# Kernel tuning notes

Measured on AMD Instinct MI355X. Metric: run time of the kernel, lower is better.

Reference implementation:

```python
import jax, jax.numpy as jnp
import numpy as np

B, S, E = 2, 4096, 1024
QD, VD = 64, 64
WIN, DIL = 5, 2


def setup_inputs() -> dict:
    key = jax.random.key(0)
    ks = jax.random.split(key, 7)
    sc = E ** -0.5  # linear-layer init scale
    return {
        "x": jax.random.normal(ks[0], (B, S, E), jnp.float32),
        "Wq": jax.random.normal(ks[1], (E, QD), jnp.float32) * sc,
        "bq": jnp.zeros((QD,), jnp.float32),
        "Wk": jax.random.normal(ks[2], (E, QD), jnp.float32) * sc,
        "bk": jnp.zeros((QD,), jnp.float32),
        "Wv": jax.random.normal(ks[3], (E, VD), jnp.float32) * sc,
        "bv": jnp.zeros((VD,), jnp.float32),
    }


def reference(x, Wq, bq, Wk, bk, Wv, bv):
    b, s, _ = x.shape
    Q = x @ Wq + bq  # (b, s, QD)
    K = x @ Wk + bk  # (b, s, QD)
    V = x @ Wv + bv  # (b, s, VD)

    half = WIN // 2
    offsets = DIL * (jnp.arange(WIN) - half)
    i = jnp.arange(s)                                  # (s,)
    j = i[None, :] + offsets[:, None]
    valid = (j >= 0) & (j < s)                         # in-range band entries
    jc = jnp.clip(j, 0, s - 1)

    Kg = K[:, jc, :]
    # per-offset diagonal dot products Q_i . K_{i+d}
    c = jnp.einsum('bsd,bwsd->bws', Q, Kg) * valid

    ib = jnp.broadcast_to(i[None, :], (WIN, s))
    # Banded score matrix, zeros off-band (as in the original: torch.zeros scatter).
    # Masked (invalid) entries add 0, so clipped index collisions are harmless.
    scores = jnp.zeros((b, s, s), x.dtype).at[:, ib, jc].add(c)

    attn = jax.nn.softmax(scores, axis=2)              # softmax over full row incl. zeros
    return attn @ V                                    # (b, s, VD)
```

## Files before the change

### kernel.cpp

```cpp
#include <hip/hip_runtime.h>
#include <hip/hip_bf16.h>

typedef __hip_bfloat16 bf16;
typedef short bf16x8 __attribute__((ext_vector_type(8)));
typedef float f32x4 __attribute__((ext_vector_type(4)));

#define S_LEN 4096
#define NBATCH 2
#define EDIM 1024
#define DDIM 64
#define MROWS (NBATCH * S_LEN)

#define GLOBAL_AS __attribute__((address_space(1)))
#define LDS_AS __attribute__((address_space(3)))

union frag_u { bf16x8 v; bf16 e[8]; };

__device__ __forceinline__ void async_ld16(const void* gp, void* lp) {
  __builtin_amdgcn_global_load_lds((const GLOBAL_AS void*)gp,
                                   (LDS_AS void*)lp, 16, 0, 0);
}

__device__ __forceinline__ void cvt_split(const float4& a, const float4& b,
                                          bf16x8& hi, bf16x8& lo) {
  float v[8] = {a.x, a.y, a.z, a.w, b.x, b.y, b.z, b.w};
  frag_u h, l;
#pragma unroll
  for (int e = 0; e < 8; e++) {
    bf16 hh = __float2bfloat16(v[e]);
    h.e[e] = hh;
    l.e[e] = __float2bfloat16(v[e] - __bfloat162float(hh));
  }
  hi = h.v;
  lo = l.v;
}

__global__ __launch_bounds__(256) void pack_w_kernel(
    const float* __restrict__ Wq, const float* __restrict__ Wk,
    const float* __restrict__ Wv, bf16* __restrict__ Wt2_hi,
    bf16* __restrict__ Wt2_lo, float* __restrict__ Vsum) {
  __shared__ float tile[64 * 65];
  const int mat = blockIdx.x >> 4;
  const int kb = blockIdx.x & 15;
  const int t = threadIdx.x;
  if (blockIdx.x == 0 && t < NBATCH * DDIM) Vsum[t] = 0.f;
  const float* W = (mat == 0) ? Wq : ((mat == 1) ? Wk : Wv);

#pragma unroll
  for (int i = 0; i < 4; i++) {
    int F = (i * 256 + t) * 4;
    int k = F >> 6;
    int n4 = F & 63;
    float4 v = *(const float4*)(const void*)(W + (size_t)(kb * 64 + k) * 64 + n4);
    tile[(n4 + 0) * 65 + k] = v.x;
    tile[(n4 + 1) * 65 + k] = v.y;
    tile[(n4 + 2) * 65 + k] = v.z;
    tile[(n4 + 3) * 65 + k] = v.w;
  }
  __syncthreads();

#pragma unroll
  for (int it = 0; it < 2; it++) {
    int uidx = it * 256 + t;
    int nl = uidx >> 3;
    int j_half = (uidx >> 2) & 1;
    int pp_k = uidx & 3;
    int ng = mat * 64 + nl;
    int n2 = ng >> 1;
    int sp = ((ng & 1) * 4 + pp_k) ^ (n2 & 7);
    int unit = n2 * 8 + sp;
    int j = kb * 2 + j_half;
    frag_u h, l;
#pragma unroll
    for (int e = 0; e < 8; e++) {
      float v = tile[nl * 65 + j_half * 32 + pp_k * 8 + e];
      bf16 hh = __float2bfloat16(v);
      h.e[e] = hh;
      l.e[e] = __float2bfloat16(v - __bfloat162float(hh));
    }
    size_t ob = (size_t)j * 6144 + unit * 8;
    *(bf16x8*)(void*)(Wt2_hi + ob) = h.v;
    *(bf16x8*)(void*)(Wt2_lo + ob) = l.v;
  }
}

__global__ __launch_bounds__(512, 2) void qkv_gemm_kernel(
    const float* __restrict__ x, const bf16* __restrict__ Wt2_hi,
    const bf16* __restrict__ Wt2_lo, const float* __restrict__ bq,
    const float* __restrict__ bk, const float* __restrict__ bv,
    float* __restrict__ qkv, float* __restrict__ Vsum) {
  __shared__ __align__(16) char lds[131072];
  const int tid = threadIdx.x;
  const int lane = tid & 63;
  const int wave = tid >> 6;
  const int nh = wave & 3;
  const int kh = wave >> 2;
  const int quad = lane >> 4;
  const int l16 = lane & 15;
  const int rowBase = blockIdx.x * 32;

  const int sp = ((l16 & 1) * 4 + quad) ^ ((l16 >> 1) & 7);
  const int loff = ((l16 >> 1) * 8 + sp) * 8;
  const bf16* bhp = Wt2_hi + (size_t)kh * 98304 + nh * 1536 + loff;
  const bf16* blp = Wt2_lo + (size_t)kh * 98304 + nh * 1536 + loff;

  bf16x8 Bh[3][3], Bl[3][3];
  f32x4 acc[2][3];
#pragma unroll
  for (int f = 0; f < 2; f++)
#pragma unroll
    for (int t = 0; t < 3; t++) acc[f][t] = (f32x4){0.f, 0.f, 0.f, 0.f};

#define LOADB(s, r)                                                          \
  {                                                                          \
    const bf16* _h = bhp + (size_t)(r) * 6144;                               \
    const bf16* _l = blp + (size_t)(r) * 6144;                               \
    Bh[s][0] = *(const bf16x8*)(const void*)(_h);                            \
    Bh[s][1] = *(const bf16x8*)(const void*)(_h + 512);                      \
    Bh[s][2] = *(const bf16x8*)(const void*)(_h + 1024);                     \
    Bl[s][0] = *(const bf16x8*)(const void*)(_l);                            \
    Bl[s][1] = *(const bf16x8*)(const void*)(_l + 512);                      \
    Bl[s][2] = *(const bf16x8*)(const void*)(_l + 1024);                     \
  }

#pragma unroll
  for (int i = 0; i < 16; i++) {
    const int Rl = (wave << 2) | (i >> 2);
    const int g = i & 3;
    const char* src = (const char*)x + (size_t)(rowBase + Rl) * 4096 +
                      (size_t)g * 1024 + ((lane ^ (Rl & 7)) << 4);
    async_ld16(src, lds + Rl * 4096 + g * 1024);
  }
  asm volatile("" ::: "memory");
  LOADB(0, 0);
  LOADB(1, 1);
  LOADB(2, 2);
  asm volatile("s_waitcnt vmcnt(18)" ::: "memory");
  __builtin_amdgcn_s_barrier();
  __builtin_amdgcn_sched_barrier(0);

  const char* aRow0 = lds + l16 * 4096;
  const char* aRow1 = lds + (16 + l16) * 4096;
  const int aE = (((quad * 2) ^ (l16 & 7)) << 4);

#pragma unroll
  for (int r = 0; r < 16; ++r) {
    const int Rk = kh * 16 + r;
    float4 a00 = *(const float4*)(const void*)(aRow0 + Rk * 128 + aE);
    float4 a01 = *(const float4*)(const void*)(aRow0 + Rk * 128 + (aE ^ 16));
    float4 a10 = *(const float4*)(const void*)(aRow1 + Rk * 128 + aE);
    float4 a11 = *(const float4*)(const void*)(aRow1 + Rk * 128 + (aE ^ 16));
    bf16x8 ah0, al0, ah1, al1;
    cvt_split(a00, a01, ah0, al0);
    cvt_split(a10, a11, ah1, al1);
    const int s = r % 3;
#pragma unroll
    for (int t = 0; t < 3; t++) {
      acc[0][t] =
          __builtin_amdgcn_mfma_f32_16x16x32_bf16(ah0, Bh[s][t], acc[0][t], 0, 0, 0);
      acc[0][t] =
          __builtin_amdgcn_mfma_f32_16x16x32_bf16(ah0, Bl[s][t], acc[0][t], 0, 0, 0);
      acc[0][t] =
          __builtin_amdgcn_mfma_f32_16x16x32_bf16(al0, Bh[s][t], acc[0][t], 0, 0, 0);
      acc[1][t] =
          __builtin_amdgcn_mfma_f32_16x16x32_bf16(ah1, Bh[s][t], acc[1][t], 0, 0, 0);
      acc[1][t] =
          __builtin_amdgcn_mfma_f32_16x16x32_bf16(ah1, Bl[s][t], acc[1][t], 0, 0, 0);
      acc[1][t] =
          __builtin_amdgcn_mfma_f32_16x16x32_bf16(al1, Bh[s][t], acc[1][t], 0, 0, 0);
    }
    if (r + 3 < 16) LOADB((r + 3) % 3, r + 3);
    asm volatile("" ::: "memory");
  }
#undef LOADB

  f32x4(*red)[64][6] = (f32x4(*)[64][6])lds;
  __syncthreads();
  if (kh == 1) {
#pragma unroll
    for (int f = 0; f < 2; f++)
#pragma unroll
      for (int t = 0; t < 3; t++) red[nh][lane][f * 3 + t] = acc[f][t];
  }
  __syncthreads();
  if (kh == 1) return;
#pragma unroll
  for (int f = 0; f < 2; f++)
#pragma unroll
    for (int t = 0; t < 3; t++) acc[f][t] += red[nh][lane][f * 3 + t];

  const int bb = rowBase >> 12;
#pragma unroll
  for (int f = 0; f < 2; f++)
#pragma unroll
    for (int t = 0; t < 3; t++) {
      int nt = nh * 3 + t;
      int n = nt * 16 + l16;
      int mat = n >> 6;
      int col = n & 63;
      float bias = (mat == 0) ? bq[col] : ((mat == 1) ? bk[col] : bv[col]);
      float* dst = qkv + (size_t)mat * MROWS * DDIM +
                   (size_t)(rowBase + f * 16 + quad * 4) * DDIM + col;
      float vs = 0.f;
#pragma unroll
      for (int rr = 0; rr < 4; rr++) {
        float val = acc[f][t][rr] + bias;
        dst[rr * DDIM] = val;
        vs += val;
      }
      if (nt >= 8) {
        vs += __shfl_xor(vs, 16, 64);
        vs += __shfl_xor(vs, 32, 64);
        if (quad == 0) atomicAdd(&Vsum[bb * DDIM + (n - 128)], vs);
      }
    }
}

__global__ __launch_bounds__(256) void attn_kernel(
    const float* __restrict__ qkv, const float* __restrict__ Vsum,
    float* __restrict__ out) {
  const float* Qf = qkv;
  const float* Kf = qkv + (size_t)MROWS * DDIM;
  const float* Vf = qkv + (size_t)2 * MROWS * DDIM;
  int l = threadIdx.x & 31;
  int qidx = blockIdx.x * 8 + (threadIdx.x >> 5);
  int b = qidx >> 12;
  int i = qidx & 4095;

  float2 q = *(const float2*)(const void*)(Qf + (size_t)qidx * DDIM + 2 * l);
  float sc[5];
  float2 vv[5];
  bool val[5];
#pragma unroll
  for (int w = 0; w < 5; w++) {
    int j = i + 2 * w - 4;
    val[w] = (j >= 0) && (j < S_LEN);
    int jj = val[w] ? j : i;
    size_t off = (size_t)(b * S_LEN + jj) * DDIM + 2 * l;
    float2 kk = *(const float2*)(const void*)(Kf + off);
    vv[w] = *(const float2*)(const void*)(Vf + off);
    float p = q.x * kk.x + q.y * kk.y;
#pragma unroll
    for (int d = 1; d < 32; d <<= 1) p += __shfl_xor(p, d, 64);
    sc[w] = p;
  }

  float mx = 0.f;
#pragma unroll
  for (int w = 0; w < 5; w++)
    if (val[w]) mx = fmaxf(mx, sc[w]);

  float denom = 0.f;
  float2 accv = {0.f, 0.f}, vsel = {0.f, 0.f};
  int nval = 0;
#pragma unroll
  for (int w = 0; w < 5; w++)
    if (val[w]) {
      float pexp = __expf(sc[w] - mx);
      denom += pexp;
      accv.x += pexp * vv[w].x;
      accv.y += pexp * vv[w].y;
      vsel.x += vv[w].x;
      vsel.y += vv[w].y;
      nval++;
    }
  float pbg = __expf(-mx);
  denom += pbg * (float)(S_LEN - nval);
  float2 vsm = *(const float2*)(const void*)(Vsum + b * DDIM + 2 * l);
  accv.x += pbg * (vsm.x - vsel.x);
  accv.y += pbg * (vsm.y - vsel.y);

  float2 o = {accv.x / denom, accv.y / denom};
  *(float2*)(void*)(out + (size_t)qidx * DDIM + 2 * l) = o;
}

extern "C" void kernel_launch(void* const* d_in, const int* in_sizes, int n_in,
                              void* d_out, int out_size, void* d_ws,
                              size_t ws_size, hipStream_t stream) {
  const float* x = (const float*)d_in[0];
  const float* Wq = (const float*)d_in[1];
  const float* bq = (const float*)d_in[2];
  const float* Wk = (const float*)d_in[3];
  const float* bk = (const float*)d_in[4];
  const float* Wv = (const float*)d_in[5];
  const float* bv = (const float*)d_in[6];
  float* out = (float*)d_out;

  char* ws = (char*)d_ws;
  bf16* Wt2_hi = (bf16*)ws;
  bf16* Wt2_lo = (bf16*)(ws + 393216);
  float* qkv = (float*)(ws + 786432);
  float* Vsum = (float*)(ws + 786432 + 6291456);

  hipLaunchKernelGGL(pack_w_kernel, dim3(48), dim3(256), 0, stream, Wq, Wk, Wv,
                     Wt2_hi, Wt2_lo, Vsum);
  hipLaunchKernelGGL(qkv_gemm_kernel, dim3(256), dim3(512), 0, stream, x,
                     Wt2_hi, Wt2_lo, bq, bk, bv, qkv, Vsum);
  hipLaunchKernelGGL(attn_kernel, dim3(1024), dim3(256), 0, stream, qkv, Vsum,
                     out);
}
```

Baseline: 106.4 us.

## Fuse weight packing, QKV GEMM and banded attention into one cooperative kernel

```diff
diff --git a/kernel.cpp b/kernel.cpp
--- a/kernel.cpp
+++ b/kernel.cpp
@@ -1,5 +1,8 @@
 #include <hip/hip_runtime.h>
 #include <hip/hip_bf16.h>
+#include <hip/hip_cooperative_groups.h>
+
+namespace cg = cooperative_groups;
 
 typedef __hip_bfloat16 bf16;
 typedef short bf16x8 __attribute__((ext_vector_type(8)));
@@ -33,6 +36,260 @@
   }
   hi = h.v;
   lo = l.v;
+}
+
+__global__ __launch_bounds__(512, 2) void fused_kernel(
+    const float* __restrict__ x, const float* __restrict__ Wq,
+    const float* __restrict__ bq, const float* __restrict__ Wk,
+    const float* __restrict__ bk, const float* __restrict__ Wv,
+    const float* __restrict__ bv, bf16* __restrict__ Wt2_hi,
+    bf16* __restrict__ Wt2_lo, float* __restrict__ qkv,
+    float* __restrict__ Vsum, float* __restrict__ out) {
+  __shared__ __align__(16) char lds[147712];
+  const int tid = threadIdx.x;
+  const int lane = tid & 63;
+  const int wave = tid >> 6;
+  const int nh = wave & 3;
+  const int kh = wave >> 2;
+  const int quad = lane >> 4;
+  const int l16 = lane & 15;
+  const int vb = ((blockIdx.x & 7) << 5) | (blockIdx.x >> 3);
+  const int rowBase = vb * 32;
+
+#pragma unroll
+  for (int i = 0; i < 16; i++) {
+    const int Rl = (wave << 2) | (i >> 2);
+    const int g = i & 3;
+    const char* src = (const char*)x + (size_t)(rowBase + Rl) * 4096 +
+                      (size_t)g * 1024 + ((lane ^ (Rl & 7)) << 4);
+    async_ld16(src, lds + Rl * 4096 + g * 1024);
+  }
+
+  if (blockIdx.x < 48) {
+    float* tile = (float*)(lds + 131072);
+    const int mat = blockIdx.x >> 4;
+    const int kb = blockIdx.x & 15;
+    const float* W = (mat == 0) ? Wq : ((mat == 1) ? Wk : Wv);
+#pragma unroll
+    for (int i2 = 0; i2 < 2; i2++) {
+      int F = (i2 * 512 + tid) * 4;
+      int k = F >> 6;
+      int n4 = F & 63;
+      float4 v =
+          *(const float4*)(const void*)(W + (size_t)(kb * 64 + k) * 64 + n4);
+      tile[(n4 + 0) * 65 + k] = v.x;
+      tile[(n4 + 1) * 65 + k] = v.y;
+      tile[(n4 + 2) * 65 + k] = v.z;
+      tile[(n4 + 3) * 65 + k] = v.w;
+    }
+    __syncthreads();
+    {
+      int nl = tid >> 3;
+      int j_half = (tid >> 2) & 1;
+      int pp_k = tid & 3;
+      int ng = mat * 64 + nl;
+      int n2 = ng >> 1;
+      int sp = ((ng & 1) * 4 + pp_k) ^ (n2 & 7);
+      int unit = n2 * 8 + sp;
+      int jp = kb * 2 + j_half;
+      frag_u h, l;
+#pragma unroll
+      for (int e = 0; e < 8; e++) {
+        float v = tile[nl * 65 + j_half * 32 + pp_k * 8 + e];
+        bf16 hh = __float2bfloat16(v);
+        h.e[e] = hh;
+        l.e[e] = __float2bfloat16(v - __bfloat162float(hh));
+      }
+      size_t ob = (size_t)jp * 6144 + unit * 8;
+      *(bf16x8*)(void*)(Wt2_hi + ob) = h.v;
+      *(bf16x8*)(void*)(Wt2_lo + ob) = l.v;
+    }
+  }
+  if (blockIdx.x == 0 && tid < NBATCH * DDIM) Vsum[tid] = 0.f;
+  __threadfence();
+  cg::this_grid().sync();
+
+  const int sp = ((l16 & 1) * 4 + quad) ^ ((l16 >> 1) & 7);
+  const int loff = ((l16 >> 1) * 8 + sp) * 8;
+  const bf16* bhp = Wt2_hi + (size_t)kh * 98304 + nh * 1536 + loff;
+  const bf16* blp = Wt2_lo + (size_t)kh * 98304 + nh * 1536 + loff;
+
+  bf16x8 Bh[3][3], Bl[3][3];
+  f32x4 acc[2][3];
+#pragma unroll
+  for (int f = 0; f < 2; f++)
+#pragma unroll
+    for (int t = 0; t < 3; t++) acc[f][t] = (f32x4){0.f, 0.f, 0.f, 0.f};
+
+#define LOADB(s, r)                                                          \
+  {                                                                          \
+    const bf16* _h = bhp + (size_t)(r) * 6144;                               \
+    const bf16* _l = blp + (size_t)(r) * 6144;                               \
+    Bh[s][0] = *(const bf16x8*)(const void*)(_h);                            \
+    Bh[s][1] = *(const bf16x8*)(const void*)(_h + 512);                      \
+    Bh[s][2] = *(const bf16x8*)(const void*)(_h + 1024);                     \
+    Bl[s][0] = *(const bf16x8*)(const void*)(_l);                            \
+    Bl[s][1] = *(const bf16x8*)(const void*)(_l + 512);                      \
+    Bl[s][2] = *(const bf16x8*)(const void*)(_l + 1024);                     \
+  }
+
+  LOADB(0, 0);
+  LOADB(1, 1);
+  LOADB(2, 2);
+  asm volatile("s_waitcnt vmcnt(18)" ::: "memory");
+  __builtin_amdgcn_s_barrier();
+  __builtin_amdgcn_sched_barrier(0);
+
+  const char* aRow0 = lds + l16 * 4096;
+  const char* aRow1 = lds + (16 + l16) * 4096;
+  const int aE = (((quad * 2) ^ (l16 & 7)) << 4);
+
+#pragma unroll
+  for (int r = 0; r < 16; ++r) {
+    const int Rk = kh * 16 + r;
+    float4 a00 = *(const float4*)(const void*)(aRow0 + Rk * 128 + aE);
+    float4 a01 = *(const float4*)(const void*)(aRow0 + Rk * 128 + (aE ^ 16));
+    float4 a10 = *(const float4*)(const void*)(aRow1 + Rk * 128 + aE);
+    float4 a11 = *(const float4*)(const void*)(aRow1 + Rk * 128 + (aE ^ 16));
+    bf16x8 ah0, al0, ah1, al1;
+    cvt_split(a00, a01, ah0, al0);
+    cvt_split(a10, a11, ah1, al1);
+    const int s = r % 3;
+#pragma unroll
+    for (int t = 0; t < 3; t++) {
+      acc[0][t] =
+          __builtin_amdgcn_mfma_f32_16x16x32_bf16(ah0, Bh[s][t], acc[0][t], 0, 0, 0);
+      acc[0][t] =
+          __builtin_amdgcn_mfma_f32_16x16x32_bf16(ah0, Bl[s][t], acc[0][t], 0, 0, 0);
+      acc[0][t] =
+          __builtin_amdgcn_mfma_f32_16x16x32_bf16(al0, Bh[s][t], acc[0][t], 0, 0, 0);
+      acc[1][t] =
+          __builtin_amdgcn_mfma_f32_16x16x32_bf16(ah1, Bh[s][t], acc[1][t], 0, 0, 0);
+      acc[1][t] =
+          __builtin_amdgcn_mfma_f32_16x16x32_bf16(ah1, Bl[s][t], acc[1][t], 0, 0, 0);
+      acc[1][t] =
+          __builtin_amdgcn_mfma_f32_16x16x32_bf16(al1, Bh[s][t], acc[1][t], 0, 0, 0);
+    }
+    if (r + 3 < 16) LOADB((r + 3) % 3, r + 3);
+    asm volatile("" ::: "memory");
+  }
+#undef LOADB
+
+  f32x4(*red)[64][6] = (f32x4(*)[64][6])lds;
+  float* ldsQ = (float*)(lds + 98304);
+  __syncthreads();
+  if (kh == 1) {
+#pragma unroll
+    for (int f = 0; f < 2; f++)
+#pragma unroll
+      for (int t = 0; t < 3; t++) red[nh][lane][f * 3 + t] = acc[f][t];
+  }
+  __syncthreads();
+  if (kh == 0) {
+#pragma unroll
+    for (int f = 0; f < 2; f++)
+#pragma unroll
+      for (int t = 0; t < 3; t++) acc[f][t] += red[nh][lane][f * 3 + t];
+    const int bb = rowBase >> 12;
+#pragma unroll
+    for (int f = 0; f < 2; f++)
+#pragma unroll
+      for (int t = 0; t < 3; t++) {
+        int nt = nh * 3 + t;
+        int n = nt * 16 + l16;
+        if (n < 64) {
+          float bias = bq[n];
+#pragma unroll
+          for (int rr = 0; rr < 4; rr++)
+            ldsQ[(f * 16 + quad * 4 + rr) * 64 + n] = acc[f][t][rr] + bias;
+        } else {
+          int mat = n >> 6;
+          int col = n & 63;
+          float bias = (mat == 1) ? bk[col] : bv[col];
+          float* dst = qkv + (size_t)mat * MROWS * DDIM +
+                       (size_t)(rowBase + f * 16 + quad * 4) * DDIM + col;
+          float vs = 0.f;
+#pragma unroll
+          for (int rr = 0; rr < 4; rr++) {
+            float val = acc[f][t][rr] + bias;
+            dst[rr * DDIM] = val;
+            vs += val;
+          }
+          if (nt >= 8) {
+            vs += __shfl_xor(vs, 16, 64);
+            vs += __shfl_xor(vs, 32, 64);
+            if (quad == 0) atomicAdd(&Vsum[bb * DDIM + (n - 128)], vs);
+          }
+        }
+      }
+  }
+  __threadfence();
+  cg::this_grid().sync();
+
+  {
+    const float* Kf = qkv + (size_t)MROWS * DDIM;
+    const float* Vf = qkv + (size_t)2 * MROWS * DDIM;
+    const int l16c = tid & 15;
+    const int qloc = tid >> 4;
+    const int qidx = rowBase + qloc;
+    const int b = qidx >> 12;
+    const int i = qidx & 4095;
+
+    float4 q = *(const float4*)(const void*)(ldsQ + qloc * 64 + 4 * l16c);
+    float sc[5];
+    float4 vv[5];
+    bool val[5];
+#pragma unroll
+    for (int w = 0; w < 5; w++) {
+      int j = i + 2 * w - 4;
+      val[w] = (j >= 0) && (j < S_LEN);
+      int jj = val[w] ? j : i;
+      size_t off = (size_t)(b * S_LEN + jj) * DDIM + 4 * l16c;
+      float4 kk = *(const float4*)(const void*)(Kf + off);
+      vv[w] = *(const float4*)(const void*)(Vf + off);
+      float p = q.x * kk.x + q.y * kk.y + q.z * kk.z + q.w * kk.w;
+      p += __shfl_xor(p, 1, 64);
+      p += __shfl_xor(p, 2, 64);
+      p += __shfl_xor(p, 4, 64);
+      p += __shfl_xor(p, 8, 64);
+      sc[w] = p;
+    }
+
+    float mx = 0.f;
+#pragma unroll
+    for (int w = 0; w < 5; w++)
+      if (val[w]) mx = fmaxf(mx, sc[w]);
+
+    float denom = 0.f;
+    float4 accv = {0.f, 0.f, 0.f, 0.f}, vsel = {0.f, 0.f, 0.f, 0.f};
+    int nval = 0;
+#pragma unroll
+    for (int w = 0; w < 5; w++)
+      if (val[w]) {
+        float pexp = __expf(sc[w] - mx);
+        denom += pexp;
+        accv.x += pexp * vv[w].x;
+        accv.y += pexp * vv[w].y;
+        accv.z += pexp * vv[w].z;
+        accv.w += pexp * vv[w].w;
+        vsel.x += vv[w].x;
+        vsel.y += vv[w].y;
+        vsel.z += vv[w].z;
+        vsel.w += vv[w].w;
+        nval++;
+      }
+    float pbg = __expf(-mx);
+    denom += pbg * (float)(S_LEN - nval);
+    float4 vsm = *(const float4*)(const void*)(Vsum + b * DDIM + 4 * l16c);
+    accv.x += pbg * (vsm.x - vsel.x);
+    accv.y += pbg * (vsm.y - vsel.y);
+    accv.z += pbg * (vsm.z - vsel.z);
+    accv.w += pbg * (vsm.w - vsel.w);
+
+    float4 o = {accv.x / denom, accv.y / denom, accv.z / denom,
+                accv.w / denom};
+    *(float4*)(void*)(out + (size_t)qidx * DDIM + 4 * l16c) = o;
+  }
 }
 
 __global__ __launch_bounds__(256) void pack_w_kernel(
@@ -292,10 +549,19 @@
   float* qkv = (float*)(ws + 786432);
   float* Vsum = (float*)(ws + 786432 + 6291456);
 
-  hipLaunchKernelGGL(pack_w_kernel, dim3(48), dim3(256), 0, stream, Wq, Wk, Wv,
-                     Wt2_hi, Wt2_lo, Vsum);
-  hipLaunchKernelGGL(qkv_gemm_kernel, dim3(256), dim3(512), 0, stream, x,
-                     Wt2_hi, Wt2_lo, bq, bk, bv, qkv, Vsum);
-  hipLaunchKernelGGL(attn_kernel, dim3(1024), dim3(256), 0, stream, qkv, Vsum,
-                     out);
-}
+  void* args[12] = {(void*)&x,      (void*)&Wq,     (void*)&bq,
+                    (void*)&Wk,     (void*)&bk,     (void*)&Wv,
+                    (void*)&bv,     (void*)&Wt2_hi, (void*)&Wt2_lo,
+                    (void*)&qkv,    (void*)&Vsum,   (void*)&out};
+  hipError_t err = hipLaunchCooperativeKernel((const void*)fused_kernel,
+                                              dim3(256), dim3(512), args, 0,
+                                              stream);
+  if (err != hipSuccess) {
+    hipLaunchKernelGGL(pack_w_kernel, dim3(48), dim3(256), 0, stream, Wq, Wk,
+                       Wv, Wt2_hi, Wt2_lo, Vsum);
+    hipLaunchKernelGGL(qkv_gemm_kernel, dim3(256), dim3(512), 0, stream, x,
+                       Wt2_hi, Wt2_lo, bq, bk, bv, qkv, Vsum);
+    hipLaunchKernelGGL(attn_kernel, dim3(1024), dim3(256), 0, stream, qkv,
+                       Vsum, out);
+  }
+}
```

Measured after the change: 277.3 us. 161% more time.

## Fuse attention into QKV GEMM with neighbor flags and precompute V column sums

Applied to the files above, without the earlier changes.

```diff
diff --git a/kernel.cpp b/kernel.cpp
--- a/kernel.cpp
+++ b/kernel.cpp
@@ -35,60 +35,95 @@
   lo = l.v;
 }
 
-__global__ __launch_bounds__(256) void pack_w_kernel(
-    const float* __restrict__ Wq, const float* __restrict__ Wk,
-    const float* __restrict__ Wv, bf16* __restrict__ Wt2_hi,
-    bf16* __restrict__ Wt2_lo, float* __restrict__ Vsum) {
-  __shared__ float tile[64 * 65];
-  const int mat = blockIdx.x >> 4;
-  const int kb = blockIdx.x & 15;
+__global__ __launch_bounds__(256) void prep_kernel(
+    const float* __restrict__ x, const float* __restrict__ Wq,
+    const float* __restrict__ Wk, const float* __restrict__ Wv,
+    bf16* __restrict__ Wt2_hi, bf16* __restrict__ Wt2_lo,
+    float* __restrict__ Vpart, int* __restrict__ flags) {
+  __shared__ float smem[64 * 65];
   const int t = threadIdx.x;
-  if (blockIdx.x == 0 && t < NBATCH * DDIM) Vsum[t] = 0.f;
-  const float* W = (mat == 0) ? Wq : ((mat == 1) ? Wk : Wv);
-
-#pragma unroll
-  for (int i = 0; i < 4; i++) {
-    int F = (i * 256 + t) * 4;
-    int k = F >> 6;
-    int n4 = F & 63;
-    float4 v = *(const float4*)(const void*)(W + (size_t)(kb * 64 + k) * 64 + n4);
-    tile[(n4 + 0) * 65 + k] = v.x;
-    tile[(n4 + 1) * 65 + k] = v.y;
-    tile[(n4 + 2) * 65 + k] = v.z;
-    tile[(n4 + 3) * 65 + k] = v.w;
-  }
-  __syncthreads();
-
-#pragma unroll
-  for (int it = 0; it < 2; it++) {
-    int uidx = it * 256 + t;
-    int nl = uidx >> 3;
-    int j_half = (uidx >> 2) & 1;
-    int pp_k = uidx & 3;
-    int ng = mat * 64 + nl;
-    int n2 = ng >> 1;
-    int sp = ((ng & 1) * 4 + pp_k) ^ (n2 & 7);
-    int unit = n2 * 8 + sp;
-    int j = kb * 2 + j_half;
-    frag_u h, l;
-#pragma unroll
-    for (int e = 0; e < 8; e++) {
-      float v = tile[nl * 65 + j_half * 32 + pp_k * 8 + e];
-      bf16 hh = __float2bfloat16(v);
-      h.e[e] = hh;
-      l.e[e] = __float2bfloat16(v - __bfloat162float(hh));
-    }
-    size_t ob = (size_t)j * 6144 + unit * 8;
-    *(bf16x8*)(void*)(Wt2_hi + ob) = h.v;
-    *(bf16x8*)(void*)(Wt2_lo + ob) = l.v;
-  }
-}
-
-__global__ __launch_bounds__(512, 2) void qkv_gemm_kernel(
+  const int bid = blockIdx.x;
+
+  if (bid < 48) {
+    if (bid == 0) flags[t] = 0;
+    const int mat = bid >> 4;
+    const int kb = bid & 15;
+    const float* W = (mat == 0) ? Wq : ((mat == 1) ? Wk : Wv);
+#pragma unroll
+    for (int i = 0; i < 4; i++) {
+      int F = (i * 256 + t) * 4;
+      int k = F >> 6;
+      int n4 = F & 63;
+      float4 v =
+          *(const float4*)(const void*)(W + (size_t)(kb * 64 + k) * 64 + n4);
+      smem[(n4 + 0) * 65 + k] = v.x;
+      smem[(n4 + 1) * 65 + k] = v.y;
+      smem[(n4 + 2) * 65 + k] = v.z;
+      smem[(n4 + 3) * 65 + k] = v.w;
+    }
+    __syncthreads();
+#pragma unroll
+    for (int it = 0; it < 2; it++) {
+      int uidx = it * 256 + t;
+      int nl = uidx >> 3;
+      int j_half = (uidx >> 2) & 1;
+      int pp_k = uidx & 3;
+      int ng = mat * 64 + nl;
+      int n2 = ng >> 1;
+      int sp = ((ng & 1) * 4 + pp_k) ^ (n2 & 7);
+      int unit = n2 * 8 + sp;
+      int j = kb * 2 + j_half;
+      frag_u h, l;
+#pragma unroll
+      for (int e = 0; e < 8; e++) {
+        float v = smem[nl * 65 + j_half * 32 + pp_k * 8 + e];
+        bf16 hh = __float2bfloat16(v);
+        h.e[e] = hh;
+        l.e[e] = __float2bfloat16(v - __bfloat162float(hh));
+      }
+      size_t ob = (size_t)j * 6144 + unit * 8;
+      *(bf16x8*)(void*)(Wt2_hi + ob) = h.v;
+      *(bf16x8*)(void*)(Wt2_lo + ob) = l.v;
+    }
+  } else {
+    const int v = bid - 48;
+    float a0 = 0.f, a1 = 0.f, a2 = 0.f, a3 = 0.f;
+    const float* xr = x + (size_t)v * 32 * EDIM + 4 * t;
+    for (int i = 0; i < 32; i++) {
+      float4 xv = *(const float4*)(const void*)(xr + (size_t)i * EDIM);
+      a0 += xv.x;
+      a1 += xv.y;
+      a2 += xv.z;
+      a3 += xv.w;
+    }
+    float* rs = smem;
+    rs[4 * t + 0] = a0;
+    rs[4 * t + 1] = a1;
+    rs[4 * t + 2] = a2;
+    rs[4 * t + 3] = a3;
+    __syncthreads();
+    const int col = t & 63;
+    const int kq = t >> 6;
+    float s = 0.f;
+    const float* wvp = Wv + (size_t)(kq * 256) * 64 + col;
+    const float* rsp = rs + kq * 256;
+#pragma unroll 8
+    for (int k8 = 0; k8 < 256; k8++) s += rsp[k8] * wvp[(size_t)k8 * 64];
+    float* part = smem + 1024;
+    part[kq * 64 + col] = s;
+    __syncthreads();
+    if (t < 64)
+      Vpart[(size_t)v * 64 + t] =
+          part[t] + part[64 + t] + part[128 + t] + part[192 + t];
+  }
+}
+
+__global__ __launch_bounds__(512, 2) void fused_main(
     const float* __restrict__ x, const bf16* __restrict__ Wt2_hi,
     const bf16* __restrict__ Wt2_lo, const float* __restrict__ bq,
     const float* __restrict__ bk, const float* __restrict__ bv,
-    float* __restrict__ qkv, float* __restrict__ Vsum) {
+    float* __restrict__ qkv, const float* __restrict__ Vpart,
+    int* __restrict__ flags, float* __restrict__ out) {
   __shared__ __align__(16) char lds[131072];
   const int tid = threadIdx.x;
   const int lane = tid & 63;
@@ -183,95 +218,131 @@
       for (int t = 0; t < 3; t++) red[nh][lane][f * 3 + t] = acc[f][t];
   }
   __syncthreads();
-  if (kh == 1) return;
-#pragma unroll
-  for (int f = 0; f < 2; f++)
-#pragma unroll
-    for (int t = 0; t < 3; t++) acc[f][t] += red[nh][lane][f * 3 + t];
-
-  const int bb = rowBase >> 12;
-#pragma unroll
-  for (int f = 0; f < 2; f++)
-#pragma unroll
-    for (int t = 0; t < 3; t++) {
-      int nt = nh * 3 + t;
-      int n = nt * 16 + l16;
-      int mat = n >> 6;
-      int col = n & 63;
-      float bias = (mat == 0) ? bq[col] : ((mat == 1) ? bk[col] : bv[col]);
-      float* dst = qkv + (size_t)mat * MROWS * DDIM +
-                   (size_t)(rowBase + f * 16 + quad * 4) * DDIM + col;
-      float vs = 0.f;
-#pragma unroll
-      for (int rr = 0; rr < 4; rr++) {
-        float val = acc[f][t][rr] + bias;
-        dst[rr * DDIM] = val;
-        vs += val;
+  if (kh == 0) {
+#pragma unroll
+    for (int f = 0; f < 2; f++)
+#pragma unroll
+      for (int t = 0; t < 3; t++) acc[f][t] += red[nh][lane][f * 3 + t];
+#pragma unroll
+    for (int f = 0; f < 2; f++)
+#pragma unroll
+      for (int t = 0; t < 3; t++) {
+        int nt = nh * 3 + t;
+        int n = nt * 16 + l16;
+        int mat = n >> 6;
+        int col = n & 63;
+        float bias = (mat == 0) ? bq[col] : ((mat == 1) ? bk[col] : bv[col]);
+        float* dst = qkv + (size_t)mat * MROWS * DDIM +
+                     (size_t)(rowBase + f * 16 + quad * 4) * DDIM + col;
+#pragma unroll
+        for (int rr = 0; rr < 4; rr++) dst[rr * DDIM] = acc[f][t][rr] + bias;
       }
-      if (nt >= 8) {
-        vs += __shfl_xor(vs, 16, 64);
-        vs += __shfl_xor(vs, 32, 64);
-        if (quad == 0) atomicAdd(&Vsum[bb * DDIM + (n - 128)], vs);
+  }
+
+  __threadfence();
+  __syncthreads();
+  if (tid == 0)
+    __hip_atomic_store(&flags[blockIdx.x], 1, __ATOMIC_RELEASE,
+                       __HIP_MEMORY_SCOPE_AGENT);
+
+  float* vs_scr = (float*)lds;
+  {
+    const int bb2 = tid >> 8;
+    const int rest = tid & 255;
+    const int ch = rest >> 6;
+    const int col = rest & 63;
+    float s = 0.f;
+    const float* vp = Vpart + (size_t)(bb2 * 128 + ch * 32) * 64 + col;
+#pragma unroll 4
+    for (int p = 0; p < 32; p++) s += vp[(size_t)p * 64];
+    vs_scr[(bb2 * 4 + ch) * 64 + col] = s;
+  }
+  __syncthreads();
+  float* Vsum_l = (float*)(lds + 4096);
+  if (tid < 128) {
+    const int bb2 = tid >> 6;
+    const int col = tid & 63;
+    Vsum_l[tid] = vs_scr[bb2 * 256 + col] + vs_scr[bb2 * 256 + 64 + col] +
+                  vs_scr[bb2 * 256 + 128 + col] +
+                  vs_scr[bb2 * 256 + 192 + col] + 4096.f * bv[col];
+  }
+
+  if (blockIdx.x > 0 && tid == 0) {
+    while (__hip_atomic_load(&flags[blockIdx.x - 1], __ATOMIC_ACQUIRE,
+                             __HIP_MEMORY_SCOPE_AGENT) == 0)
+      __builtin_amdgcn_s_sleep(2);
+  }
+  __syncthreads();
+
+  {
+    const float* Kf = qkv + (size_t)MROWS * DDIM;
+    const float* Vf = qkv + (size_t)2 * MROWS * DDIM;
+    const int l16c = tid & 15;
+    const int qloc = tid >> 4;
+    const int qstart = (blockIdx.x == 0) ? 0 : rowBase - 16;
+    const int qend = (blockIdx.x == 255) ? MROWS : rowBase + 16;
+    for (int q0 = qstart; q0 < qend; q0 += 32) {
+      const int qidx = q0 + qloc;
+      const bool live = qidx < qend;
+      const int qc = live ? qidx : (qend - 1);
+      const int bb2 = qc >> 12;
+      const int i = qc & 4095;
+      float4 q4 =
+          *(const float4*)(const void*)(qkv + (size_t)qc * DDIM + 4 * l16c);
+      float sc[5];
+      float4 vv[5];
+      bool val[5];
+#pragma unroll
+      for (int w = 0; w < 5; w++) {
+        int j = i + 2 * w - 4;
+        val[w] = (j >= 0) && (j < S_LEN);
+        int jj = val[w] ? j : i;
+        size_t off = (size_t)(bb2 * S_LEN + jj) * DDIM + 4 * l16c;
+        float4 kk = *(const float4*)(const void*)(Kf + off);
+        vv[w] = *(const float4*)(const void*)(Vf + off);
+        float p = q4.x * kk.x + q4.y * kk.y + q4.z * kk.z + q4.w * kk.w;
+        p += __shfl_xor(p, 1, 64);
+        p += __shfl_xor(p, 2, 64);
+        p += __shfl_xor(p, 4, 64);
+        p += __shfl_xor(p, 8, 64);
+        sc[w] = p;
       }
-    }
-}
-
-__global__ __launch_bounds__(256) void attn_kernel(
-    const float* __restrict__ qkv, const float* __restrict__ Vsum,
-    float* __restrict__ out) {
-  const float* Qf = qkv;
-  const float* Kf = qkv + (size_t)MROWS * DDIM;
-  const float* Vf = qkv + (size_t)2 * MROWS * DDIM;
-  int l = threadIdx.x & 31;
-  int qidx = blockIdx.x * 8 + (threadIdx.x >> 5);
-  int b = qidx >> 12;
-  int i = qidx & 4095;
-
-  float2 q = *(const float2*)(const void*)(Qf + (size_t)qidx * DDIM + 2 * l);
-  float sc[5];
-  float2 vv[5];
-  bool val[5];
-#pragma unroll
-  for (int w = 0; w < 5; w++) {
-    int j = i + 2 * w - 4;
-    val[w] = (j >= 0) && (j < S_LEN);
-    int jj = val[w] ? j : i;
-    size_t off = (size_t)(b * S_LEN + jj) * DDIM + 2 * l;
-    float2 kk = *(const float2*)(const void*)(Kf + off);
-    vv[w] = *(const float2*)(const void*)(Vf + off);
-    float p = q.x * kk.x + q.y * kk.y;
-#pragma unroll
-    for (int d = 1; d < 32; d <<= 1) p += __shfl_xor(p, d, 64);
-    sc[w] = p;
-  }
-
-  float mx = 0.f;
-#pragma unroll
-  for (int w = 0; w < 5; w++)
-    if (val[w]) mx = fmaxf(mx, sc[w]);
-
-  float denom = 0.f;
-  float2 accv = {0.f, 0.f}, vsel = {0.f, 0.f};
-  int nval = 0;
-#pragma unroll
-  for (int w = 0; w < 5; w++)
-    if (val[w]) {
-      float pexp = __expf(sc[w] - mx);
-      denom += pexp;
-      accv.x += pexp * vv[w].x;
-      accv.y += pexp * vv[w].y;
-      vsel.x += vv[w].x;
-      vsel.y += vv[w].y;
-      nval++;
-    }
-  float pbg = __expf(-mx);
-  denom += pbg * (float)(S_LEN - nval);
-  float2 vsm = *(const float2*)(const void*)(Vsum + b * DDIM + 2 * l);
-  accv.x += pbg * (vsm.x - vsel.x);
-  accv.y += pbg * (vsm.y - vsel.y);
-
-  float2 o = {accv.x / denom, accv.y / denom};
-  *(float2*)(void*)(out + (size_t)qidx * DDIM + 2 * l) = o;
+      float mx = 0.f;
+#pragma unroll
+      for (int w = 0; w < 5; w++)
+        if (val[w]) mx = fmaxf(mx, sc[w]);
+      float denom = 0.f;
+      float4 accv = {0.f, 0.f, 0.f, 0.f}, vsel = {0.f, 0.f, 0.f, 0.f};
+      int nval = 0;
+#pragma unroll
+      for (int w = 0; w < 5; w++)
+        if (val[w]) {
+          float pexp = __expf(sc[w] - mx);
+          denom += pexp;
+          accv.x += pexp * vv[w].x;
+          accv.y += pexp * vv[w].y;
+          accv.z += pexp * vv[w].z;
+          accv.w += pexp * vv[w].w;
+          vsel.x += vv[w].x;
+          vsel.y += vv[w].y;
+          vsel.z += vv[w].z;
+          vsel.w += vv[w].w;
+          nval++;
+        }
+      float pbg = __expf(-mx);
+      denom += pbg * (float)(S_LEN - nval);
+      float4 vsm =
+          *(const float4*)(const void*)(Vsum_l + bb2 * 64 + 4 * l16c);
+      accv.x += pbg * (vsm.x - vsel.x);
+      accv.y += pbg * (vsm.y - vsel.y);
+      accv.z += pbg * (vsm.z - vsel.z);
+      accv.w += pbg * (vsm.w - vsel.w);
+      float4 o = {accv.x / denom, accv.y / denom, accv.z / denom,
+                  accv.w / denom};
+      if (live)
+        *(float4*)(void*)(out + (size_t)qidx * DDIM + 4 * l16c) = o;
+    }
+  }
 }
 
 extern "C" void kernel_launch(void* const* d_in, const int* in_sizes, int n_in,
@@ -290,12 +361,11 @@
   bf16* Wt2_hi = (bf16*)ws;
   bf16* Wt2_lo = (bf16*)(ws + 393216);
   float* qkv = (float*)(ws + 786432);
-  float* Vsum = (float*)(ws + 786432 + 6291456);
-
-  hipLaunchKernelGGL(pack_w_kernel, dim3(48), dim3(256), 0, stream, Wq, Wk, Wv,
-                     Wt2_hi, Wt2_lo, Vsum);
-  hipLaunchKernelGGL(qkv_gemm_kernel, dim3(256), dim3(512), 0, stream, x,
-                     Wt2_hi, Wt2_lo, bq, bk, bv, qkv, Vsum);
-  hipLaunchKernelGGL(attn_kernel, dim3(1024), dim3(256), 0, stream, qkv, Vsum,
-                     out);
-}
+  float* Vpart = (float*)(ws + 7077888);
+  int* flags = (int*)(ws + 7143424);
+
+  hipLaunchKernelGGL(prep_kernel, dim3(304), dim3(256), 0, stream, x, Wq, Wk,
+                     Wv, Wt2_hi, Wt2_lo, Vpart, flags);
+  hipLaunchKernelGGL(fused_main, dim3(256), dim3(512), 0, stream, x, Wt2_hi,
+                     Wt2_lo, bq, bk, bv, qkv, Vpart, flags, out);
+}
```

New measurement: 153.0 us. 1.44x slower.

## Split GEMM A-tile staging to overlap load with compute; vectorize attention lanes

Applied to the files above, without the earlier changes.

```diff
diff --git a/kernel.cpp b/kernel.cpp
--- a/kernel.cpp
+++ b/kernel.cpp
@@ -122,15 +122,13 @@
     Bl[s][1] = *(const bf16x8*)(const void*)(_l + 512);                      \
     Bl[s][2] = *(const bf16x8*)(const void*)(_l + 1024);                     \
   }
-
-#pragma unroll
-  for (int i = 0; i < 16; i++) {
-    const int Rl = (wave << 2) | (i >> 2);
-    const int g = i & 3;
-    const char* src = (const char*)x + (size_t)(rowBase + Rl) * 4096 +
-                      (size_t)g * 1024 + ((lane ^ (Rl & 7)) << 4);
-    async_ld16(src, lds + Rl * 4096 + g * 1024);
-  }
+#define ADMA(Rl, g)                                                          \
+  async_ld16((const char*)x + (size_t)(rowBase + (Rl)) * 4096 +              \
+                 (size_t)(g) * 1024 + ((lane ^ ((Rl) & 7)) << 4),            \
+             lds + (Rl) * 4096 + (g) * 1024)
+
+#pragma unroll
+  for (int i = 0; i < 8; i++) ADMA((wave << 2) | (i >> 1), (i & 1) * 2);
   asm volatile("" ::: "memory");
   LOADB(0, 0);
   LOADB(1, 1);
@@ -143,35 +141,55 @@
   const char* aRow1 = lds + (16 + l16) * 4096;
   const int aE = (((quad * 2) ^ (l16 & 7)) << 4);
 
-#pragma unroll
-  for (int r = 0; r < 16; ++r) {
-    const int Rk = kh * 16 + r;
-    float4 a00 = *(const float4*)(const void*)(aRow0 + Rk * 128 + aE);
-    float4 a01 = *(const float4*)(const void*)(aRow0 + Rk * 128 + (aE ^ 16));
-    float4 a10 = *(const float4*)(const void*)(aRow1 + Rk * 128 + aE);
-    float4 a11 = *(const float4*)(const void*)(aRow1 + Rk * 128 + (aE ^ 16));
-    bf16x8 ah0, al0, ah1, al1;
-    cvt_split(a00, a01, ah0, al0);
-    cvt_split(a10, a11, ah1, al1);
-    const int s = r % 3;
-#pragma unroll
-    for (int t = 0; t < 3; t++) {
-      acc[0][t] =
-          __builtin_amdgcn_mfma_f32_16x16x32_bf16(ah0, Bh[s][t], acc[0][t], 0, 0, 0);
-      acc[0][t] =
-          __builtin_amdgcn_mfma_f32_16x16x32_bf16(ah0, Bl[s][t], acc[0][t], 0, 0, 0);
-      acc[0][t] =
-          __builtin_amdgcn_mfma_f32_16x16x32_bf16(al0, Bh[s][t], acc[0][t], 0, 0, 0);
-      acc[1][t] =
-          __builtin_amdgcn_mfma_f32_16x16x32_bf16(ah1, Bh[s][t], acc[1][t], 0, 0, 0);
-      acc[1][t] =
-          __builtin_amdgcn_mfma_f32_16x16x32_bf16(ah1, Bl[s][t], acc[1][t], 0, 0, 0);
-      acc[1][t] =
-          __builtin_amdgcn_mfma_f32_16x16x32_bf16(al1, Bh[s][t], acc[1][t], 0, 0, 0);
+#define COMPUTE(r)                                                           \
+  {                                                                          \
+    const int Rk = kh * 16 + (r);                                            \
+    float4 a00 = *(const float4*)(const void*)(aRow0 + Rk * 128 + aE);       \
+    float4 a01 = *(const float4*)(const void*)(aRow0 + Rk * 128 + (aE ^ 16));\
+    float4 a10 = *(const float4*)(const void*)(aRow1 + Rk * 128 + aE);       \
+    float4 a11 = *(const float4*)(const void*)(aRow1 + Rk * 128 + (aE ^ 16));\
+    bf16x8 ah0, al0, ah1, al1;                                               \
+    cvt_split(a00, a01, ah0, al0);                                           \
+    cvt_split(a10, a11, ah1, al1);                                           \
+    const int s = (r) % 3;                                                   \
+    _Pragma("unroll") for (int t = 0; t < 3; t++) {                          \
+      acc[0][t] = __builtin_amdgcn_mfma_f32_16x16x32_bf16(ah0, Bh[s][t],     \
+                                                          acc[0][t], 0, 0, 0);\
+      acc[0][t] = __builtin_amdgcn_mfma_f32_16x16x32_bf16(ah0, Bl[s][t],     \
+                                                          acc[0][t], 0, 0, 0);\
+      acc[0][t] = __builtin_amdgcn_mfma_f32_16x16x32_bf16(al0, Bh[s][t],     \
+                                                          acc[0][t], 0, 0, 0);\
+      acc[1][t] = __builtin_amdgcn_mfma_f32_16x16x32_bf16(ah1, Bh[s][t],     \
+                                                          acc[1][t], 0, 0, 0);\
+      acc[1][t] = __builtin_amdgcn_mfma_f32_16x16x32_bf16(ah1, Bl[s][t],     \
+                                                          acc[1][t], 0, 0, 0);\
+      acc[1][t] = __builtin_amdgcn_mfma_f32_16x16x32_bf16(al1, Bh[s][t],     \
+                                                          acc[1][t], 0, 0, 0);\
+    }                                                                        \
+  }
+
+#pragma unroll
+  for (int r = 0; r < 8; ++r) {
+    COMPUTE(r);
+    LOADB((r + 3) % 3, r + 3);
+    if (r < 4) {
+      ADMA((wave << 2) | r, 1);
+      ADMA((wave << 2) | r, 3);
     }
+    asm volatile("" ::: "memory");
+  }
+  asm volatile("s_waitcnt vmcnt(18)" ::: "memory");
+  __builtin_amdgcn_s_barrier();
+  __builtin_amdgcn_sched_barrier(0);
+
+#pragma unroll
+  for (int r = 8; r < 16; ++r) {
+    COMPUTE(r);
     if (r + 3 < 16) LOADB((r + 3) % 3, r + 3);
     asm volatile("" ::: "memory");
   }
+#undef COMPUTE
+#undef ADMA
 #undef LOADB
 
   f32x4(*red)[64][6] = (f32x4(*)[64][6])lds;
@@ -222,26 +240,28 @@
   const float* Qf = qkv;
   const float* Kf = qkv + (size_t)MROWS * DDIM;
   const float* Vf = qkv + (size_t)2 * MROWS * DDIM;
-  int l = threadIdx.x & 31;
-  int qidx = blockIdx.x * 8 + (threadIdx.x >> 5);
-  int b = qidx >> 12;
-  int i = qidx & 4095;
-
-  float2 q = *(const float2*)(const void*)(Qf + (size_t)qidx * DDIM + 2 * l);
+  const int l16c = threadIdx.x & 15;
+  const int qidx = blockIdx.x * 16 + (threadIdx.x >> 4);
+  const int b = qidx >> 12;
+  const int i = qidx & 4095;
+
+  float4 q = *(const float4*)(const void*)(Qf + (size_t)qidx * DDIM + 4 * l16c);
   float sc[5];
-  float2 vv[5];
+  float4 vv[5];
   bool val[5];
 #pragma unroll
   for (int w = 0; w < 5; w++) {
     int j = i + 2 * w - 4;
     val[w] = (j >= 0) && (j < S_LEN);
     int jj = val[w] ? j : i;
-    size_t off = (size_t)(b * S_LEN + jj) * DDIM + 2 * l;
-    float2 kk = *(const float2*)(const void*)(Kf + off);
-    vv[w] = *(const float2*)(const void*)(Vf + off);
-    float p = q.x * kk.x + q.y * kk.y;
-#pragma unroll
-    for (int d = 1; d < 32; d <<= 1) p += __shfl_xor(p, d, 64);
+    size_t off = (size_t)(b * S_LEN + jj) * DDIM + 4 * l16c;
+    float4 kk = *(const float4*)(const void*)(Kf + off);
+    vv[w] = *(const float4*)(const void*)(Vf + off);
+    float p = q.x * kk.x + q.y * kk.y + q.z * kk.z + q.w * kk.w;
+    p += __shfl_xor(p, 1, 64);
+    p += __shfl_xor(p, 2, 64);
+    p += __shfl_xor(p, 4, 64);
+    p += __shfl_xor(p, 8, 64);
     sc[w] = p;
   }
 
@@ -251,7 +271,7 @@
     if (val[w]) mx = fmaxf(mx, sc[w]);
 
   float denom = 0.f;
-  float2 accv = {0.f, 0.f}, vsel = {0.f, 0.f};
+  float4 accv = {0.f, 0.f, 0.f, 0.f}, vsel = {0.f, 0.f, 0.f, 0.f};
   int nval = 0;
 #pragma unroll
   for (int w = 0; w < 5; w++)
@@ -260,18 +280,24 @@
       denom += pexp;
       accv.x += pexp * vv[w].x;
       accv.y += pexp * vv[w].y;
+      accv.z += pexp * vv[w].z;
+      accv.w += pexp * vv[w].w;
       vsel.x += vv[w].x;
       vsel.y += vv[w].y;
+      vsel.z += vv[w].z;
+      vsel.w += vv[w].w;
       nval++;
     }
   float pbg = __expf(-mx);
   denom += pbg * (float)(S_LEN - nval);
-  float2 vsm = *(const float2*)(const void*)(Vsum + b * DDIM + 2 * l);
+  float4 vsm = *(const float4*)(const void*)(Vsum + b * DDIM + 4 * l16c);
   accv.x += pbg * (vsm.x - vsel.x);
   accv.y += pbg * (vsm.y - vsel.y);
-
-  float2 o = {accv.x / denom, accv.y / denom};
-  *(float2*)(void*)(out + (size_t)qidx * DDIM + 2 * l) = o;
+  accv.z += pbg * (vsm.z - vsel.z);
+  accv.w += pbg * (vsm.w - vsel.w);
+
+  float4 o = {accv.x / denom, accv.y / denom, accv.z / denom, accv.w / denom};
+  *(float4*)(void*)(out + (size_t)qidx * DDIM + 4 * l16c) = o;
 }
 
 extern "C" void kernel_launch(void* const* d_in, const int* in_sizes, int n_in,
@@ -296,6 +322,6 @@
                      Wt2_hi, Wt2_lo, Vsum);
   hipLaunchKernelGGL(qkv_gemm_kernel, dim3(256), dim3(512), 0, stream, x,
                      Wt2_hi, Wt2_lo, bq, bk, bv, qkv, Vsum);
-  hipLaunchKernelGGL(attn_kernel, dim3(1024), dim3(256), 0, stream, qkv, Vsum,
+  hipLaunchKernelGGL(attn_kernel, dim3(512), dim3(256), 0, stream, qkv, Vsum,
                      out);
 }
```

After: 105.5 us. No clear change (-0.8%).
